# Kernel tuning notes

Hardware: AMD Instinct MI355X
Metric: run time of the kernel (lower is better)

The kernel has to match this reference:

```python
import jax, jax.numpy as jnp
import numpy as np

NFFT = 4_194_304
NMODES = 2
NTAPS = 101
GAMMA = 0.0016567  # [/W/m]
DZ = 80000.0       # [m]


def setup_inputs() -> dict:
    key = jax.random.key(0)
    k1, k2, k3 = jax.random.split(key, 3)
    xr = jax.random.normal(k1, (NFFT, NMODES), dtype=jnp.float32)
    xi = jax.random.normal(k2, (NFFT, NMODES), dtype=jnp.float32)
    # fconv1d kernel: [ntaps, in_features=Nmodes, out_features=Nmodes] (lecun_normal-ish scale)
    W = jax.random.normal(k3, (NTAPS, NMODES, NMODES), dtype=jnp.float32) / np.sqrt(NTAPS * NMODES)
    b = jnp.zeros((NMODES,), dtype=jnp.float32)
    power = jnp.zeros((1,), dtype=jnp.float32)  # 0 dBm
    return {"xr": xr, "xi": xi, "W": W, "b": b, "power": power}


def reference(xr, xi, W, b, power):
    # P = |x|^2, shape [Nfft, Nmodes]
    P = xr * xr + xi * xi
    # valid 1D conv over time: [Nfft, Nmodes] -> [Nfft - ntaps + 1, Nmodes]
    phi = jax.lax.conv_general_dilated(
        P[None],            # [1, Nfft, Nmodes]
        W,                  # [ntaps, in, out]
        window_strides=(1,),
        padding='VALID',
        dimension_numbers=('NWC', 'WIO', 'NWC'),
    )[0] + b                # [Nfft - ntaps + 1, Nmodes]

    nmodes = xr.shape[-1]
    scale = 0.001 * 10.0 ** (power[0] / 10.0) / nmodes  # dBm -> W, per mode
    n0 = NTAPS // 2
    x = (xr + 1j * xi)[n0:xr.shape[0] - n0]  # valid-conv aligned slice
    y = x * jnp.exp(-1j * phi * (GAMMA * scale * DZ))
    return y
```

## Files before the change

kernel.cpp:

```cpp
#include <hip/hip_runtime.h>
#include <hip/hip_bf16.h>

#define NFFT   4194304
#define NMODES 2
#define NTAPS  101
#define NVALID (NFFT - NTAPS + 1)
#define N0     (NTAPS / 2)

constexpr int BLOCK = 256;
constexpr int TILE  = 2048;
constexpr int NT    = (NVALID + TILE - 1) / TILE;
constexpr int WIN   = 2176;
constexpr int NM    = 15;
constexpr int TBW   = 272;

typedef __attribute__((ext_vector_type(8)))  short short8;
typedef __attribute__((ext_vector_type(16))) float float16;

static __device__ __forceinline__ unsigned short f2bf(float x) {
    __hip_bfloat16 h = __float2bfloat16(x);
    return *reinterpret_cast<unsigned short*>(&h);
}
static __device__ __forceinline__ unsigned pk(float e0, float e1) {
    return (unsigned)f2bf(e0) | ((unsigned)f2bf(e1) << 16);
}
static __device__ __forceinline__ int swz(int s) {
    return s ^ (((s >> 5) & 7) << 2);
}

__global__ __launch_bounds__(BLOCK, 8) void nl_kernel(
    const float* __restrict__ xa,
    const float* __restrict__ xb,
    const float* __restrict__ W,  const float* __restrict__ b,
    const float* __restrict__ power, unsigned* __restrict__ out)
{
    __shared__ __align__(16) unsigned Pl[WIN];
    __shared__ __align__(16) unsigned Bt[TBW];

    const int tid  = threadIdx.x;
    const int lane = tid & 63;
    const int wid  = tid >> 6;
    const int colc = lane & 31;
    const int h    = lane >> 5;
    const int cs   = colc >> 1;
    const int o    = colc & 1;
    const int r    = colc;

    const int tile_start = blockIdx.x * TILE;

    const float4* __restrict__ xa4 = reinterpret_cast<const float4*>(xa);
    const float4* __restrict__ xb4 = reinterpret_cast<const float4*>(xb);
    #pragma unroll
    for (int k = 0; k < 5; ++k) {
        const int s = 2 * tid + 512 * k;
        if (k < 4 || s < WIN) {
            const int g = tile_start + s;
            float4 a = make_float4(0.f, 0.f, 0.f, 0.f), c = a;
            if (g < NFFT) { a = xa4[g >> 1]; c = xb4[g >> 1]; }
            const unsigned u0 = pk(a.x * a.x + c.x * c.x, a.y * a.y + c.y * c.y);
            const unsigned u1 = pk(a.z * a.z + c.z * c.z, a.w * a.w + c.w * c.w);
            *reinterpret_cast<uint2*>(&Pl[swz(s)]) = make_uint2(u0, u1);
        }
    }

    __builtin_amdgcn_sched_barrier(0);

    {
        const float4* __restrict__ Wt = reinterpret_cast<const float4*>(W);
        #pragma unroll
        for (int idx = tid; idx < TBW; idx += BLOCK) {
            const int t  = (idx >> 1) - 15;
            const int oo = idx & 1;
            const bool ok = (unsigned)t <= 100u;
            const float4 w = Wt[ok ? t : 0];
            Bt[idx] = ok ? pk(oo ? w.y : w.x, oo ? w.w : w.z) : 0u;
        }
    }
    __builtin_amdgcn_sched_barrier(0);
    __syncthreads();

    const int cb    = wid * 512;
    const int bbase = ((4 * h - cs + 15) << 1) | o;
    float16 acc = {};
    uint4 areg[4];
    #pragma unroll
    for (int m = 0; m < 4; ++m)
        areg[m] = *reinterpret_cast<const uint4*>(&Pl[swz(cb + 16 * r + 8 * m + 4 * h)]);
    #pragma unroll
    for (int m = 0; m < NM; ++m) {
        uint4 bq;
        bq.x = Bt[bbase + 16 * m + 0];
        bq.y = Bt[bbase + 16 * m + 2];
        bq.z = Bt[bbase + 16 * m + 4];
        bq.w = Bt[bbase + 16 * m + 6];
        acc = __builtin_amdgcn_mfma_f32_32x32x16_bf16(
                  __builtin_bit_cast(short8, areg[m & 3]),
                  __builtin_bit_cast(short8, bq), acc, 0, 0, 0);
        if (m + 4 < NM)
            areg[m & 3] = *reinterpret_cast<const uint4*>(
                              &Pl[swz(cb + 16 * r + 8 * (m + 4) + 4 * h)]);
    }

    const float bo   = o ? b[1] : b[0];
    const float coef = 0.066268f * exp10f(power[0] * 0.1f);
    #pragma unroll
    for (int j = 0; j < 16; ++j) {
        const int row = (j & 3) + 8 * (j >> 2) + 4 * h;
        const int n   = tile_start + cb + 16 * row + cs;
        if (n < NVALID) {
            const float Ax = xa[(n + N0) * 2 + o];
            const float Bx = xb[(n + N0) * 2 + o];
            float sn, cn;
            __sincosf((acc[j] + bo) * coef, &sn, &cn);
            const unsigned ov = pk(Bx * cn - Ax * sn, Ax * cn + Bx * sn);
            __builtin_nontemporal_store(ov, &out[n * 2 + o]);
        }
    }
}

extern "C" void kernel_launch(void* const* d_in, const int* in_sizes, int n_in,
                              void* d_out, int out_size, void* d_ws, size_t ws_size,
                              hipStream_t stream) {
    const float* big[2] = {nullptr, nullptr};
    const float* W = nullptr; const float* b = nullptr; const float* power = nullptr;
    int nbig = 0;
    for (int i = 0; i < n_in; ++i) {
        const float* p = (const float*)d_in[i];
        const int sz = in_sizes[i];
        if (sz == NFFT * NMODES)       { if (nbig < 2) big[nbig++] = p; }
        else if (sz == NTAPS * NMODES * NMODES) { W = p; }
        else if (sz == NMODES)         { b = p; }
        else if (sz == 1)              { power = p; }
    }

    unsigned* out = (unsigned*)d_out;
    nl_kernel<<<NT, BLOCK, 0, stream>>>(big[0], big[1], W, b, power, out);
}
```

Measured before the change: 121.9 us.

## Transpose MFMA accumulators through LDS for vectorized epilogue loads and stores

The accumulator phase values are written into shared memory (reusing the P and weight region) and read back so that each thread owns eight consecutive time samples. The epilogue can then load the x inputs as float4 and store the output as 16-byte nontemporal vectors, replacing the scattered 4-byte loads and stores of the MFMA output layout. The last tile keeps a guarded scalar path. This costs two extra block barriers and an LDS round trip, and the LDS footprint grows to 16 KB, which may reduce occupancy.

```diff
diff --git a/kernel.cpp b/kernel.cpp
--- a/kernel.cpp
+++ b/kernel.cpp
@@ -16,6 +16,7 @@
 
 typedef __attribute__((ext_vector_type(8)))  short short8;
 typedef __attribute__((ext_vector_type(16))) float float16;
+typedef __attribute__((ext_vector_type(4)))  unsigned uintv4;
 
 static __device__ __forceinline__ unsigned short f2bf(float x) {
     __hip_bfloat16 h = __float2bfloat16(x);
@@ -34,8 +35,10 @@
     const float* __restrict__ W,  const float* __restrict__ b,
     const float* __restrict__ power, unsigned* __restrict__ out)
 {
-    __shared__ __align__(16) unsigned Pl[WIN];
-    __shared__ __align__(16) unsigned Bt[TBW];
+    __shared__ __align__(16) unsigned lds[4096];
+    unsigned* const Pl = lds;
+    unsigned* const Bt = lds + WIN;
+    float*    const Ph = reinterpret_cast<float*>(lds);
 
     const int tid  = threadIdx.x;
     const int lane = tid & 63;
@@ -101,20 +104,73 @@
                               &Pl[swz(cb + 16 * r + 8 * (m + 4) + 4 * h)]);
     }
 
-    const float bo   = o ? b[1] : b[0];
-    const float coef = 0.066268f * exp10f(power[0] * 0.1f);
+    const float bo = o ? b[1] : b[0];
+    __syncthreads();
     #pragma unroll
     for (int j = 0; j < 16; ++j) {
         const int row = (j & 3) + 8 * (j >> 2) + 4 * h;
-        const int n   = tile_start + cb + 16 * row + cs;
-        if (n < NVALID) {
-            const float Ax = xa[(n + N0) * 2 + o];
-            const float Bx = xb[(n + N0) * 2 + o];
-            float sn, cn;
-            __sincosf((acc[j] + bo) * coef, &sn, &cn);
-            const unsigned ov = pk(Bx * cn - Ax * sn, Ax * cn + Bx * sn);
-            __builtin_nontemporal_store(ov, &out[n * 2 + o]);
-        }
+        Ph[swz(wid * 1024 + 32 * row + colc)] = acc[j] + bo;
+    }
+    __syncthreads();
+
+    const float coef = 0.066268f * exp10f(power[0] * 0.1f);
+    const float4 f0 = *reinterpret_cast<const float4*>(&Ph[swz(16 * tid +  0)]);
+    const float4 f1 = *reinterpret_cast<const float4*>(&Ph[swz(16 * tid +  4)]);
+    const float4 f2 = *reinterpret_cast<const float4*>(&Ph[swz(16 * tid +  8)]);
+    const float4 f3 = *reinterpret_cast<const float4*>(&Ph[swz(16 * tid + 12)]);
+
+    const int base = tile_start + 8 * tid;
+    uintv4* __restrict__ out4 = reinterpret_cast<uintv4*>(out);
+
+    if (blockIdx.x != NT - 1) {
+        #define EPI(q, F) {                                                         \
+            const float4 A = xa4[((base + N0) >> 1) + (q)];                         \
+            const float4 B = xb4[((base + N0) >> 1) + (q)];                         \
+            float s00, c00, s01, c01, s10, c10, s11, c11;                           \
+            __sincosf(F.x * coef, &s00, &c00);                                      \
+            __sincosf(F.y * coef, &s01, &c01);                                      \
+            __sincosf(F.z * coef, &s10, &c10);                                      \
+            __sincosf(F.w * coef, &s11, &c11);                                      \
+            uintv4 ov;                                                              \
+            ov.x = pk(B.x * c00 - A.x * s00, A.x * c00 + B.x * s00);                \
+            ov.y = pk(B.y * c01 - A.y * s01, A.y * c01 + B.y * s01);                \
+            ov.z = pk(B.z * c10 - A.z * s10, A.z * c10 + B.z * s10);                \
+            ov.w = pk(B.w * c11 - A.w * s11, A.w * c11 + B.w * s11);                \
+            __builtin_nontemporal_store(ov, &out4[(base >> 1) + (q)]); }
+        EPI(0, f0)
+        EPI(1, f1)
+        EPI(2, f2)
+        EPI(3, f3)
+        #undef EPI
+    } else {
+        const float2* __restrict__ xa2 = reinterpret_cast<const float2*>(xa);
+        const float2* __restrict__ xb2 = reinterpret_cast<const float2*>(xb);
+        #define TEPI(q, p0v, p1v, p2v, p3v) {                                       \
+            const int n0v = base + 2 * (q);                                         \
+            if (n0v < NVALID) {                                                     \
+                const float2 Av = xa2[n0v + N0]; const float2 Bv = xb2[n0v + N0];   \
+                float s0, c0v, s1, c1v;                                             \
+                __sincosf((p0v) * coef, &s0, &c0v);                                 \
+                __sincosf((p1v) * coef, &s1, &c1v);                                 \
+                uint2 ov;                                                           \
+                ov.x = pk(Bv.x * c0v - Av.x * s0, Av.x * c0v + Bv.x * s0);          \
+                ov.y = pk(Bv.y * c1v - Av.y * s1, Av.y * c1v + Bv.y * s1);          \
+                reinterpret_cast<uint2*>(out)[n0v] = ov; }                          \
+            const int n1v = base + 2 * (q) + 1;                                     \
+            if (n1v < NVALID) {                                                     \
+                const float2 Av = xa2[n1v + N0]; const float2 Bv = xb2[n1v + N0];   \
+                float s0, c0v, s1, c1v;                                             \
+                __sincosf((p2v) * coef, &s0, &c0v);                                 \
+                __sincosf((p3v) * coef, &s1, &c1v);                                 \
+                uint2 ov;                                                           \
+                ov.x = pk(Bv.x * c0v - Av.x * s0, Av.x * c0v + Bv.x * s0);          \
+                ov.y = pk(Bv.y * c1v - Av.y * s1, Av.y * c1v + Bv.y * s1);          \
+                reinterpret_cast<uint2*>(out)[n1v] = ov; } }
+        TEPI(0, f0.x, f0.y, f0.z, f0.w)
+        TEPI(1, f1.x, f1.y, f1.z, f1.w)
+        TEPI(2, f2.x, f2.y, f2.z, f2.w)
+        TEPI(3, f3.x, f3.y, f3.z, f3.w)
+        #undef TEPI
     }
 }
 
```

New measurement: 144.5 us. 1.19x slower.

## Give each wave a private LDS window and drop the block barrier

Applied to the files above, without the earlier changes.

Each wave now loads and converts its own 640-sample power window plus a private copy of the bf16 tap table into a per-wave LDS slice. This removes the block-wide __syncthreads, so waves can start their MFMA loop as soon as their own data is ready. The cost is redundant global loads for the overlapping halo (640 vs 512 samples per wave), four copies of the weight table, and more LDS per block. The epilogue bounds check is also hoisted so only the last block tests n < NVALID.

```diff
diff --git a/kernel.cpp b/kernel.cpp
--- a/kernel.cpp
+++ b/kernel.cpp
@@ -8,11 +8,13 @@
 #define N0     (NTAPS / 2)
 
 constexpr int BLOCK = 256;
+constexpr int WTILE = 512;
 constexpr int TILE  = 2048;
 constexpr int NT    = (NVALID + TILE - 1) / TILE;
-constexpr int WIN   = 2176;
+constexpr int WWIN  = 640;
 constexpr int NM    = 15;
 constexpr int TBW   = 272;
+constexpr int WLDS  = WWIN + TBW;
 
 typedef __attribute__((ext_vector_type(8)))  short short8;
 typedef __attribute__((ext_vector_type(16))) float float16;
@@ -34,8 +36,7 @@
     const float* __restrict__ W,  const float* __restrict__ b,
     const float* __restrict__ power, unsigned* __restrict__ out)
 {
-    __shared__ __align__(16) unsigned Pl[WIN];
-    __shared__ __align__(16) unsigned Bt[TBW];
+    __shared__ __align__(16) unsigned lds[4 * WLDS];
 
     const int tid  = threadIdx.x;
     const int lane = tid & 63;
@@ -46,21 +47,22 @@
     const int o    = colc & 1;
     const int r    = colc;
 
-    const int tile_start = blockIdx.x * TILE;
+    unsigned* const Pl = lds + wid * WLDS;
+    unsigned* const Bt = Pl + WWIN;
+
+    const int wstart = blockIdx.x * TILE + wid * WTILE;
 
     const float4* __restrict__ xa4 = reinterpret_cast<const float4*>(xa);
     const float4* __restrict__ xb4 = reinterpret_cast<const float4*>(xb);
     #pragma unroll
     for (int k = 0; k < 5; ++k) {
-        const int s = 2 * tid + 512 * k;
-        if (k < 4 || s < WIN) {
-            const int g = tile_start + s;
-            float4 a = make_float4(0.f, 0.f, 0.f, 0.f), c = a;
-            if (g < NFFT) { a = xa4[g >> 1]; c = xb4[g >> 1]; }
-            const unsigned u0 = pk(a.x * a.x + c.x * c.x, a.y * a.y + c.y * c.y);
-            const unsigned u1 = pk(a.z * a.z + c.z * c.z, a.w * a.w + c.w * c.w);
-            *reinterpret_cast<uint2*>(&Pl[swz(s)]) = make_uint2(u0, u1);
-        }
+        const int s = 2 * lane + 128 * k;
+        const int g = wstart + s;
+        float4 a = make_float4(0.f, 0.f, 0.f, 0.f), c = a;
+        if (g < NFFT) { a = xa4[g >> 1]; c = xb4[g >> 1]; }
+        const unsigned u0 = pk(a.x * a.x + c.x * c.x, a.y * a.y + c.y * c.y);
+        const unsigned u1 = pk(a.z * a.z + c.z * c.z, a.w * a.w + c.w * c.w);
+        *reinterpret_cast<uint2*>(&Pl[swz(s)]) = make_uint2(u0, u1);
     }
 
     __builtin_amdgcn_sched_barrier(0);
@@ -68,7 +70,7 @@
     {
         const float4* __restrict__ Wt = reinterpret_cast<const float4*>(W);
         #pragma unroll
-        for (int idx = tid; idx < TBW; idx += BLOCK) {
+        for (int idx = lane; idx < TBW; idx += 64) {
             const int t  = (idx >> 1) - 15;
             const int oo = idx & 1;
             const bool ok = (unsigned)t <= 100u;
@@ -77,15 +79,13 @@
         }
     }
     __builtin_amdgcn_sched_barrier(0);
-    __syncthreads();
 
-    const int cb    = wid * 512;
     const int bbase = ((4 * h - cs + 15) << 1) | o;
     float16 acc = {};
     uint4 areg[4];
     #pragma unroll
     for (int m = 0; m < 4; ++m)
-        areg[m] = *reinterpret_cast<const uint4*>(&Pl[swz(cb + 16 * r + 8 * m + 4 * h)]);
+        areg[m] = *reinterpret_cast<const uint4*>(&Pl[swz(16 * r + 8 * m + 4 * h)]);
     #pragma unroll
     for (int m = 0; m < NM; ++m) {
         uint4 bq;
@@ -98,22 +98,37 @@
                   __builtin_bit_cast(short8, bq), acc, 0, 0, 0);
         if (m + 4 < NM)
             areg[m & 3] = *reinterpret_cast<const uint4*>(
-                              &Pl[swz(cb + 16 * r + 8 * (m + 4) + 4 * h)]);
+                              &Pl[swz(16 * r + 8 * (m + 4) + 4 * h)]);
     }
 
     const float bo   = o ? b[1] : b[0];
     const float coef = 0.066268f * exp10f(power[0] * 0.1f);
-    #pragma unroll
-    for (int j = 0; j < 16; ++j) {
-        const int row = (j & 3) + 8 * (j >> 2) + 4 * h;
-        const int n   = tile_start + cb + 16 * row + cs;
-        if (n < NVALID) {
+
+    if (blockIdx.x != NT - 1) {
+        #pragma unroll
+        for (int j = 0; j < 16; ++j) {
+            const int row = (j & 3) + 8 * (j >> 2) + 4 * h;
+            const int n   = wstart + 16 * row + cs;
             const float Ax = xa[(n + N0) * 2 + o];
             const float Bx = xb[(n + N0) * 2 + o];
             float sn, cn;
             __sincosf((acc[j] + bo) * coef, &sn, &cn);
-            const unsigned ov = pk(Bx * cn - Ax * sn, Ax * cn + Bx * sn);
-            __builtin_nontemporal_store(ov, &out[n * 2 + o]);
+            __builtin_nontemporal_store(pk(Bx * cn - Ax * sn, Ax * cn + Bx * sn),
+                                        &out[n * 2 + o]);
+        }
+    } else {
+        #pragma unroll
+        for (int j = 0; j < 16; ++j) {
+            const int row = (j & 3) + 8 * (j >> 2) + 4 * h;
+            const int n   = wstart + 16 * row + cs;
+            if (n < NVALID) {
+                const float Ax = xa[(n + N0) * 2 + o];
+                const float Bx = xb[(n + N0) * 2 + o];
+                float sn, cn;
+                __sincosf((acc[j] + bo) * coef, &sn, &cn);
+                __builtin_nontemporal_store(pk(Bx * cn - Ax * sn, Ax * cn + Bx * sn),
+                                            &out[n * 2 + o]);
+            }
         }
     }
 }
```

After: 124.3 us. No clear change (+2.0%).

## Stage raw input tiles in LDS via direct global-to-LDS loads and reuse them in epilogue

Applied to the files above, without the earlier changes.

Raw xa/xb tile windows are now loaded straight into shared memory with global_load_lds, and the power values are computed from LDS. The epilogue reads the complex samples from the staged copy instead of issuing a second round of global loads. A fast path drops the bounds check for every block except the last. The intent is to remove the duplicate global reads of the input, at the cost of much more LDS per block (about 44 KB), an extra barrier, and lower occupancy (launch bounds drop from 8 to 3).

```diff
diff --git a/kernel.cpp b/kernel.cpp
--- a/kernel.cpp
+++ b/kernel.cpp
@@ -11,8 +11,15 @@
 constexpr int TILE  = 2048;
 constexpr int NT    = (NVALID + TILE - 1) / TILE;
 constexpr int WIN   = 2176;
+constexpr int NCH   = WIN / 2;
 constexpr int NM    = 15;
 constexpr int TBW   = 272;
+
+constexpr int OXA = 0;
+constexpr int OXB = 4352;
+constexpr int OPL = 8704;
+constexpr int OBT = 10880;
+constexpr int LWORDS = 11152;
 
 typedef __attribute__((ext_vector_type(8)))  short short8;
 typedef __attribute__((ext_vector_type(16))) float float16;
@@ -27,15 +34,23 @@
 static __device__ __forceinline__ int swz(int s) {
     return s ^ (((s >> 5) & 7) << 2);
 }
+static __device__ __forceinline__ void gl16(const float4* g, unsigned* l) {
+    __builtin_amdgcn_global_load_lds(
+        (const __attribute__((address_space(1))) void*)g,
+        (__attribute__((address_space(3))) void*)l, 16, 0, 0);
+}
 
-__global__ __launch_bounds__(BLOCK, 8) void nl_kernel(
+__global__ __launch_bounds__(BLOCK, 3) void nl_kernel(
     const float* __restrict__ xa,
     const float* __restrict__ xb,
     const float* __restrict__ W,  const float* __restrict__ b,
     const float* __restrict__ power, unsigned* __restrict__ out)
 {
-    __shared__ __align__(16) unsigned Pl[WIN];
-    __shared__ __align__(16) unsigned Bt[TBW];
+    __shared__ __align__(16) unsigned lds[LWORDS];
+    unsigned* const xaR = lds + OXA;
+    unsigned* const xbR = lds + OXB;
+    unsigned* const Pl  = lds + OPL;
+    unsigned* const Bt  = lds + OBT;
 
     const int tid  = threadIdx.x;
     const int lane = tid & 63;
@@ -47,20 +62,22 @@
     const int r    = colc;
 
     const int tile_start = blockIdx.x * TILE;
+    const int ts2        = tile_start >> 1;
 
     const float4* __restrict__ xa4 = reinterpret_cast<const float4*>(xa);
     const float4* __restrict__ xb4 = reinterpret_cast<const float4*>(xb);
     #pragma unroll
-    for (int k = 0; k < 5; ++k) {
-        const int s = 2 * tid + 512 * k;
-        if (k < 4 || s < WIN) {
-            const int g = tile_start + s;
-            float4 a = make_float4(0.f, 0.f, 0.f, 0.f), c = a;
-            if (g < NFFT) { a = xa4[g >> 1]; c = xb4[g >> 1]; }
-            const unsigned u0 = pk(a.x * a.x + c.x * c.x, a.y * a.y + c.y * c.y);
-            const unsigned u1 = pk(a.z * a.z + c.z * c.z, a.w * a.w + c.w * c.w);
-            *reinterpret_cast<uint2*>(&Pl[swz(s)]) = make_uint2(u0, u1);
-        }
+    for (int k = 0; k < 4; ++k) {
+        const int c  = tid + 256 * k;
+        const int cc = min(ts2 + c, NFFT / 2 - 1);
+        gl16(xa4 + cc, &xaR[4 * c]);
+        gl16(xb4 + cc, &xbR[4 * c]);
+    }
+    if (tid < 64) {
+        const int c  = tid + 1024;
+        const int cc = min(ts2 + c, NFFT / 2 - 1);
+        gl16(xa4 + cc, &xaR[4 * c]);
+        gl16(xb4 + cc, &xbR[4 * c]);
     }
 
     __builtin_amdgcn_sched_barrier(0);
@@ -76,7 +93,23 @@
             Bt[idx] = ok ? pk(oo ? w.y : w.x, oo ? w.w : w.z) : 0u;
         }
     }
-    __builtin_amdgcn_sched_barrier(0);
+    __syncthreads();
+
+    #pragma unroll
+    for (int k = 0; k < 5; ++k) {
+        const int tp = tid + 256 * k;
+        if (k < 4 || tp < NCH) {
+            const float4 a = *reinterpret_cast<const float4*>(&xaR[4 * tp]);
+            const float4 c = *reinterpret_cast<const float4*>(&xbR[4 * tp]);
+            const int g = tile_start + 2 * tp;
+            unsigned u0 = 0u, u1 = 0u;
+            if (g < NFFT) {
+                u0 = pk(a.x * a.x + c.x * c.x, a.y * a.y + c.y * c.y);
+                u1 = pk(a.z * a.z + c.z * c.z, a.w * a.w + c.w * c.w);
+            }
+            *reinterpret_cast<uint2*>(&Pl[swz(2 * tp)]) = make_uint2(u0, u1);
+        }
+    }
     __syncthreads();
 
     const int cb    = wid * 512;
@@ -103,17 +136,36 @@
 
     const float bo   = o ? b[1] : b[0];
     const float coef = 0.066268f * exp10f(power[0] * 0.1f);
-    #pragma unroll
-    for (int j = 0; j < 16; ++j) {
-        const int row = (j & 3) + 8 * (j >> 2) + 4 * h;
-        const int n   = tile_start + cb + 16 * row + cs;
-        if (n < NVALID) {
-            const float Ax = xa[(n + N0) * 2 + o];
-            const float Bx = xb[(n + N0) * 2 + o];
+    const float* __restrict__ xaF = reinterpret_cast<const float*>(xaR);
+    const float* __restrict__ xbF = reinterpret_cast<const float*>(xbR);
+
+    if (blockIdx.x != NT - 1) {
+        #pragma unroll
+        for (int j = 0; j < 16; ++j) {
+            const int row = (j & 3) + 8 * (j >> 2) + 4 * h;
+            const int lw  = 2 * (cb + 16 * row + cs + N0) + o;
+            const float Ax = xaF[lw];
+            const float Bx = xbF[lw];
             float sn, cn;
             __sincosf((acc[j] + bo) * coef, &sn, &cn);
-            const unsigned ov = pk(Bx * cn - Ax * sn, Ax * cn + Bx * sn);
-            __builtin_nontemporal_store(ov, &out[n * 2 + o]);
+            const int n = tile_start + cb + 16 * row + cs;
+            __builtin_nontemporal_store(pk(Bx * cn - Ax * sn, Ax * cn + Bx * sn),
+                                        &out[n * 2 + o]);
+        }
+    } else {
+        #pragma unroll
+        for (int j = 0; j < 16; ++j) {
+            const int row = (j & 3) + 8 * (j >> 2) + 4 * h;
+            const int n   = tile_start + cb + 16 * row + cs;
+            if (n < NVALID) {
+                const int lw  = 2 * (cb + 16 * row + cs + N0) + o;
+                const float Ax = xaF[lw];
+                const float Bx = xbF[lw];
+                float sn, cn;
+                __sincosf((acc[j] + bo) * coef, &sn, &cn);
+                __builtin_nontemporal_store(pk(Bx * cn - Ax * sn, Ax * cn + Bx * sn),
+                                            &out[n * 2 + o]);
+            }
         }
     }
 }
```

Result: faster. 112.8 us (-7.5%).
